# Optimization experiments

Measured on AMD Instinct MI355X. Metric: run time of the kernel, lower is better.

## Reference

```python
import jax, jax.numpy as jnp
import numpy as np

N_NODES = 100000
N_EDGES = 1600000
FEAT = 128
HID = 128
CLASSES = 10
GRAPHS = 64


def gcn_conv(x, W, b, src, dst, n):
    # PyG GCNConv: h = x @ W; add self-loops; symmetric deg^{-1/2} norm; scatter-add; + bias
    h = x @ W
    src_f = jnp.concatenate([src, jnp.arange(n, dtype=src.dtype)])
    dst_f = jnp.concatenate([dst, jnp.arange(n, dtype=dst.dtype)])
    deg = jax.ops.segment_sum(jnp.ones_like(dst_f, dtype=h.dtype), dst_f, num_segments=n)
    dinv = jax.lax.rsqrt(jnp.where(deg > 0, deg, 1.0))
    norm = dinv[src_f] * dinv[dst_f]              # [E+N]
    msg = h[src_f] * norm[:, None]                # gather + scale
    out = jax.ops.segment_sum(msg, dst_f, num_segments=n)  # scatter-add
    return out + b


def global_mean_pool(x, batch, num_graphs):
    s = jax.ops.segment_sum(x, batch, num_segments=num_graphs)
    cnt = jax.ops.segment_sum(jnp.ones_like(batch, dtype=x.dtype), batch, num_segments=num_graphs)
    return s / jnp.maximum(cnt, 1.0)[:, None]


def setup_inputs() -> dict:
    key = jax.random.key(0)
    ks = jax.random.split(key, 10)
    x = jax.random.normal(ks[0], (N_NODES, FEAT), dtype=jnp.float32)
    edge_index = jax.random.randint(ks[1], (2, N_EDGES), 0, N_NODES, dtype=jnp.int64)
    batch = jnp.sort(jax.random.randint(ks[2], (N_NODES,), 0, GRAPHS, dtype=jnp.int64))
    def glorot(k, fi, fo):
        s = float(np.sqrt(6.0 / (fi + fo)))
        return jax.random.uniform(k, (fi, fo), jnp.float32, -s, s)
    return {
        "x": x, "edge_index": edge_index, "batch": batch,
        "W1": glorot(ks[3], FEAT, HID), "b1": jnp.zeros((HID,), jnp.float32),
        "W2": glorot(ks[4], HID, HID), "b2": jnp.zeros((HID,), jnp.float32),
        "W3": glorot(ks[5], HID, HID), "b3": jnp.zeros((HID,), jnp.float32),
        "Wlin": glorot(ks[6], HID, CLASSES), "blin": jnp.zeros((CLASSES,), jnp.float32),
    }


def reference(x, edge_index, batch, W1, b1, W2, b2, W3, b3, Wlin, blin):
    src, dst = edge_index[0], edge_index[1]
    n = x.shape[0]
    h = jax.nn.relu(gcn_conv(x, W1, b1, src, dst, n))
    h = jax.nn.relu(gcn_conv(h, W2, b2, src, dst, n))
    h = gcn_conv(h, W3, b3, src, dst, n)
    emb = global_mean_pool(h, batch, GRAPHS)      # [GRAPHS, HID]
    # dropout(p=0.5) is identity in eval mode
    logits = emb @ Wlin + blin                    # [GRAPHS, CLASSES]
    return logits, jnp.squeeze(emb)
```

## Files before the change

kernel.cpp:

```cpp
#include <hip/hip_runtime.h>
#include <hip/hip_bf16.h>
#include <stdint.h>

typedef unsigned int uint32;
typedef __attribute__((ext_vector_type(8))) short short8;
typedef __attribute__((ext_vector_type(4))) float float4v;
typedef __attribute__((ext_vector_type(2))) float f32x2;

#define FEAT 128
#define NGRAPH 64
#define GB   256
#define NBK  512
#define QPG  8

__device__ __forceinline__ float bf2f_lo(uint32 v) {
    union { uint32 i; float f; } u; u.i = v << 16; return u.f;
}
__device__ __forceinline__ float bf2f_hi(uint32 v) {
    union { uint32 i; float f; } u; u.i = v & 0xffff0000u; return u.f;
}
__device__ __forceinline__ unsigned short f2bf(float f) {
    uint32 u = __builtin_bit_cast(uint32, f);
    uint32 r = (u + 0x7fffu + ((u >> 16) & 1u)) >> 16;
    return (unsigned short)r;
}
__device__ __forceinline__ uint32 f2bf2(float lo, float hi) {
    return (uint32)f2bf(lo) | ((uint32)f2bf(hi) << 16);
}

__global__ void k_bhist(const int* __restrict__ dst, int* __restrict__ bhistT,
                        const float* __restrict__ W1, const float* __restrict__ W2,
                        const float* __restrict__ W3, unsigned short* __restrict__ o1,
                        unsigned short* __restrict__ o2, unsigned short* __restrict__ o3,
                        int E) {
    int t = threadIdx.x, blk = blockIdx.x;
    if (blk >= GB) {
        int b2 = blk - GB;
        int wid = b2 >> 3;
        const float* W = (wid == 0) ? W1 : (wid == 1) ? W2 : W3;
        unsigned short* out = (wid == 0) ? o1 : (wid == 1) ? o2 : o3;
        int e = (b2 & 7) * 256 + t;
        int kt = e >> 9, ct = (e >> 6) & 7, lane = e & 63;
        int krow = kt * 32 + (lane >> 4) * 8;
        int col = ct * 16 + (lane & 15);
#pragma unroll
        for (int j = 0; j < 8; j++)
            out[e * 8 + j] = f2bf(W[(krow + j) * FEAT + col]);
        return;
    }
    __shared__ int h[NBK];
    for (int b = t; b < NBK; b += 256) h[b] = 0;
    __syncthreads();
    int chunk = (E + GB - 1) / GB;
    int lo = blk * chunk, hi = min(lo + chunk, E);
    for (int e = lo + t; e < hi; e += 256)
        atomicAdd(&h[dst[e] >> 8], 1);
    __syncthreads();
    for (int b = t; b < NBK; b += 256) bhistT[b * GB + blk] = h[b];
}

__global__ void k_boffs_a(int* __restrict__ bhistT, int* __restrict__ btot) {
    int b = blockIdx.x, l = threadIdx.x;
    int v[4];
    int base = b * GB + l * 4;
#pragma unroll
    for (int j = 0; j < 4; j++) v[j] = bhistT[base + j];
    int s = v[0] + v[1] + v[2] + v[3];
    int incl = s;
    for (int off = 1; off < 64; off <<= 1) {
        int u = __shfl_up(incl, off);
        if (l >= off) incl += u;
    }
    int excl = incl - s;
    int p0 = excl, p1 = p0 + v[0], p2 = p1 + v[1], p3 = p2 + v[2];
    bhistT[base + 0] = p0; bhistT[base + 1] = p1;
    bhistT[base + 2] = p2; bhistT[base + 3] = p3;
    if (l == 63) btot[b] = incl;
}

__global__ void k_boffs_b(const int* __restrict__ btot, int* __restrict__ bbase) {
    __shared__ int sc[NBK];
    int t = threadIdx.x;
    int s = btot[t];
    sc[t] = s;
    __syncthreads();
    for (int off = 1; off < NBK; off <<= 1) {
        int v = (t >= off) ? sc[t - off] : 0;
        __syncthreads();
        sc[t] += v;
        __syncthreads();
    }
    bbase[t] = sc[t] - s;
    if (t == NBK - 1) bbase[NBK] = sc[t];
}

__global__ void k_bscat(const int* __restrict__ src, const int* __restrict__ dst,
                        const int* __restrict__ bhistT, const int* __restrict__ bbase,
                        uint32* __restrict__ ebuf, int E) {
    __shared__ int cur[NBK];
    int t = threadIdx.x, blk = blockIdx.x;
    for (int b = t; b < NBK; b += 256) cur[b] = bbase[b] + bhistT[b * GB + blk];
    __syncthreads();
    int chunk = (E + GB - 1) / GB;
    int lo = blk * chunk, hi = min(lo + chunk, E);
    for (int e = lo + t; e < hi; e += 256) {
        int d = dst[e], s = src[e];
        int b = d >> 8;
        int p = atomicAdd(&cur[b], 1);
        ebuf[p] = ((uint32)s << 8) | (uint32)(d & 255);
    }
}

__global__ void k_csr(const uint32* __restrict__ ebuf, const int* __restrict__ bbase,
                      float* __restrict__ dinv, int* __restrict__ rowp,
                      int* __restrict__ csrc, int N, int E) {
    __shared__ int h[256];
    __shared__ int cur[256];
    int t = threadIdx.x, b = blockIdx.x;
    h[t] = 0;
    __syncthreads();
    int e0 = bbase[b], e1 = bbase[b + 1];
    for (int e = e0 + t; e < e1; e += 256)
        atomicAdd(&h[ebuf[e] & 255u], 1);
    __syncthreads();
    int deg = h[t];
    cur[t] = deg;
    __syncthreads();
    for (int off = 1; off < 256; off <<= 1) {
        int v = (t >= off) ? cur[t - off] : 0;
        __syncthreads();
        cur[t] += v;
        __syncthreads();
    }
    int r = bbase[b] + cur[t] - deg;
    int node = b * 256 + t;
    if (node < N) {
        rowp[node] = r;
        dinv[node] = rsqrtf((float)deg + 1.0f);
    }
    if (b == 0 && t == 0) rowp[N] = E;
    cur[t] = r;
    __syncthreads();
    for (int e = e0 + t; e < e1; e += 256) {
        uint32 v = ebuf[e];
        int p = atomicAdd(&cur[v & 255u], 1);
        csrc[p] = (int)(v >> 8);
    }
}

template <bool F32IN>
__global__ void k_gemm(const void* __restrict__ Xp,
                       const unsigned short* __restrict__ Wswz,
                       const float* __restrict__ dinv,
                       unsigned short* __restrict__ Hb, int N) {
    __shared__ unsigned short Wl[FEAT * FEAT];
    {
        const uint4* Wg = (const uint4*)Wswz;
        uint4* Ws = (uint4*)Wl;
        for (int i = threadIdx.x; i < 2048; i += 256) Ws[i] = Wg[i];
    }
    __syncthreads();

    int wave = threadIdx.x >> 6, lane = threadIdx.x & 63;
    int r0 = (blockIdx.x * 4 + wave) * 16;
    if (r0 >= N) return;
    int m = lane & 15, q = lane >> 4;

    int arow = r0 + m; if (arow >= N) arow = N - 1;
    short8 a[4];
    if (F32IN) {
        const float* Ar = (const float*)Xp + (long)arow * FEAT;
#pragma unroll
        for (int kt = 0; kt < 4; kt++) {
            float4 u = *(const float4*)(Ar + kt * 32 + q * 8);
            float4 v = *(const float4*)(Ar + kt * 32 + q * 8 + 4);
            short8 tv;
            tv[0] = (short)f2bf(u.x); tv[1] = (short)f2bf(u.y);
            tv[2] = (short)f2bf(u.z); tv[3] = (short)f2bf(u.w);
            tv[4] = (short)f2bf(v.x); tv[5] = (short)f2bf(v.y);
            tv[6] = (short)f2bf(v.z); tv[7] = (short)f2bf(v.w);
            a[kt] = tv;
        }
    } else {
        const short8* Ar = (const short8*)((const unsigned short*)Xp + (long)arow * FEAT);
#pragma unroll
        for (int kt = 0; kt < 4; kt++) a[kt] = Ar[kt * 4 + q];
    }

    const short8* Bl = (const short8*)Wl;
    float4v acc[8];
#pragma unroll
    for (int ct = 0; ct < 8; ct++) acc[ct] = (float4v){0.f, 0.f, 0.f, 0.f};
#pragma unroll
    for (int ct = 0; ct < 8; ct++) {
        acc[ct] = __builtin_amdgcn_mfma_f32_16x16x32_bf16(Bl[(0 * 8 + ct) * 64 + lane], a[0], acc[ct], 0, 0, 0);
        acc[ct] = __builtin_amdgcn_mfma_f32_16x16x32_bf16(Bl[(1 * 8 + ct) * 64 + lane], a[1], acc[ct], 0, 0, 0);
        acc[ct] = __builtin_amdgcn_mfma_f32_16x16x32_bf16(Bl[(2 * 8 + ct) * 64 + lane], a[2], acc[ct], 0, 0, 0);
        acc[ct] = __builtin_amdgcn_mfma_f32_16x16x32_bf16(Bl[(3 * 8 + ct) * 64 + lane], a[3], acc[ct], 0, 0, 0);
    }

    int node = r0 + m;
    bool ok = (node < N);
    float d = ok ? dinv[node] : 0.f;
#pragma unroll
    for (int ct = 0; ct < 8; ct++) {
        if (ok) {
            uint2 o;
            o.x = f2bf2(acc[ct][0] * d, acc[ct][1] * d);
            o.y = f2bf2(acc[ct][2] * d, acc[ct][3] * d);
            ((uint2*)(Hb + (long)node * FEAT + ct * 16))[q] = o;
        }
    }
}

template <int RELU>
__global__ void k_agg(const uint32* __restrict__ Hb,
                      const int* __restrict__ rowp, const int* __restrict__ csrc,
                      const float* __restrict__ dinv, const float* __restrict__ bias,
                      uint32* __restrict__ OUTb, int N) {
    int wave = threadIdx.x >> 6, lane = threadIdx.x & 63;
    int i = blockIdx.x * 4 + wave;
    if (i >= N) return;
    int f = lane & 15, quarter = lane >> 4;
    const uint4* H4 = (const uint4*)Hb;
    f32x2 c0 = {0.f, 0.f}, c1 = c0, c2 = c0, c3 = c0;
    int e0 = rowp[i], e1 = rowp[i + 1];
    int e = e0;
    for (; e + 16 <= e1; e += 16) {
        int  s[4];
        uint4 h[4];
#pragma unroll
        for (int j = 0; j < 4; j++) s[j] = csrc[e + 4 * j + quarter];
#pragma unroll
        for (int j = 0; j < 4; j++) h[j] = H4[(long)s[j] * 16 + f];
#pragma unroll
        for (int j = 0; j < 4; j++) {
            f32x2 u;
            u.x = bf2f_lo(h[j].x); u.y = bf2f_hi(h[j].x); c0 += u;
            u.x = bf2f_lo(h[j].y); u.y = bf2f_hi(h[j].y); c1 += u;
            u.x = bf2f_lo(h[j].z); u.y = bf2f_hi(h[j].z); c2 += u;
            u.x = bf2f_lo(h[j].w); u.y = bf2f_hi(h[j].w); c3 += u;
        }
    }
    {
        int r = e1 - e;
        int  s[4];
        uint4 h[4];
#pragma unroll
        for (int j = 0; j < 4; j++) {
            int idx = 4 * j + quarter;
            if (idx < r) s[j] = csrc[e + idx];
        }
#pragma unroll
        for (int j = 0; j < 4; j++)
            if (4 * j + quarter < r) h[j] = H4[(long)s[j] * 16 + f];
#pragma unroll
        for (int j = 0; j < 4; j++)
            if (4 * j + quarter < r) {
                f32x2 u;
                u.x = bf2f_lo(h[j].x); u.y = bf2f_hi(h[j].x); c0 += u;
                u.x = bf2f_lo(h[j].y); u.y = bf2f_hi(h[j].y); c1 += u;
                u.x = bf2f_lo(h[j].z); u.y = bf2f_hi(h[j].z); c2 += u;
                u.x = bf2f_lo(h[j].w); u.y = bf2f_hi(h[j].w); c3 += u;
            }
    }
    c0.x += __shfl_xor(c0.x, 16); c0.y += __shfl_xor(c0.y, 16);
    c1.x += __shfl_xor(c1.x, 16); c1.y += __shfl_xor(c1.y, 16);
    c2.x += __shfl_xor(c2.x, 16); c2.y += __shfl_xor(c2.y, 16);
    c3.x += __shfl_xor(c3.x, 16); c3.y += __shfl_xor(c3.y, 16);
    c0.x += __shfl_xor(c0.x, 32); c0.y += __shfl_xor(c0.y, 32);
    c1.x += __shfl_xor(c1.x, 32); c1.y += __shfl_xor(c1.y, 32);
    c2.x += __shfl_xor(c2.x, 32); c2.y += __shfl_xor(c2.y, 32);
    c3.x += __shfl_xor(c3.x, 32); c3.y += __shfl_xor(c3.y, 32);
    if (quarter == 0) {
        uint4 hv = H4[(long)i * 16 + f];
        c0.x += bf2f_lo(hv.x); c0.y += bf2f_hi(hv.x);
        c1.x += bf2f_lo(hv.y); c1.y += bf2f_hi(hv.y);
        c2.x += bf2f_lo(hv.z); c2.y += bf2f_hi(hv.z);
        c3.x += bf2f_lo(hv.w); c3.y += bf2f_hi(hv.w);
        float di = dinv[i];
        const float4* b4 = (const float4*)bias;
        float4 bb0 = b4[2 * f], bb1 = b4[2 * f + 1];
        c0.x = c0.x * di + bb0.x; c0.y = c0.y * di + bb0.y;
        c1.x = c1.x * di + bb0.z; c1.y = c1.y * di + bb0.w;
        c2.x = c2.x * di + bb1.x; c2.y = c2.y * di + bb1.y;
        c3.x = c3.x * di + bb1.z; c3.y = c3.y * di + bb1.w;
        if (RELU) {
            c0.x = fmaxf(c0.x, 0.f); c0.y = fmaxf(c0.y, 0.f);
            c1.x = fmaxf(c1.x, 0.f); c1.y = fmaxf(c1.y, 0.f);
            c2.x = fmaxf(c2.x, 0.f); c2.y = fmaxf(c2.y, 0.f);
            c3.x = fmaxf(c3.x, 0.f); c3.y = fmaxf(c3.y, 0.f);
        }
        uint4 o;
        o.x = f2bf2(c0.x, c0.y);
        o.y = f2bf2(c1.x, c1.y);
        o.z = f2bf2(c2.x, c2.y);
        o.w = f2bf2(c3.x, c3.y);
        ((uint4*)OUTb)[(long)i * 16 + f] = o;
    }
}

__global__ void k_pool2(const uint32* __restrict__ Gb, const int* __restrict__ batch,
                        float* __restrict__ pool, int N) {
    __shared__ float spx[256], spy[256];
    int t = threadIdx.x;
    int g = blockIdx.x >> 3, qtr = blockIdx.x & (QPG - 1);
    int lo, hi;
    { int l = 0, h = N; while (l < h) { int m = (l + h) >> 1; if (batch[m] < g) l = m + 1; else h = m; } lo = l; }
    { int l = lo, h = N; while (l < h) { int m = (l + h) >> 1; if (batch[m] < g + 1) l = m + 1; else h = m; } hi = l; }
    int cnt = hi - lo;
    int chunk = (cnt + QPG - 1) / QPG;
    int lo2 = lo + qtr * chunk;
    int hi2 = min(lo2 + chunk, hi);
    int f = t & 63, sub = t >> 6;
    float ax = 0.f, ay = 0.f;
#pragma unroll 4
    for (int i = lo2 + sub; i < hi2; i += 4) {
        uint32 v = Gb[(long)i * 64 + f];
        ax += bf2f_lo(v); ay += bf2f_hi(v);
    }
    spx[t] = ax; spy[t] = ay;
    __syncthreads();
    if (t < 64) {
        float sx = spx[t] + spx[t + 64] + spx[t + 128] + spx[t + 192];
        float sy = spy[t] + spy[t + 64] + spy[t + 128] + spy[t + 192];
        float* pr = pool + ((size_t)qtr * NGRAPH + g) * FEAT;
        pr[2 * t]     = sx;
        pr[2 * t + 1] = sy;
    }
}

__global__ void k_final(const float* __restrict__ pool, const int* __restrict__ batch,
                        const float* __restrict__ Wlin, const float* __restrict__ blin,
                        float* __restrict__ out, int N) {
    __shared__ float es[FEAT];
    __shared__ int lohi[2];
    int g = blockIdx.x, t = threadIdx.x;
    if (t < 2) {
        int key = g + t;
        int lo = 0, hi = N;
        while (lo < hi) {
            int mid = (lo + hi) >> 1;
            if (batch[mid] < key) lo = mid + 1; else hi = mid;
        }
        lohi[t] = lo;
    }
    float s = 0.f;
#pragma unroll
    for (int r = 0; r < QPG; r++) s += pool[(r * NGRAPH + g) * FEAT + t];
    __syncthreads();
    float c = (float)max(lohi[1] - lohi[0], 1);
    float e = s / c;
    es[t] = e;
    out[NGRAPH * 10 + g * FEAT + t] = e;
    __syncthreads();
    if (t < 10) {
        float a = blin[t];
        for (int k = 0; k < FEAT; k++)
            a += es[k] * Wlin[k * 10 + t];
        out[g * 10 + t] = a;
    }
}

extern "C" void kernel_launch(void* const* d_in, const int* in_sizes, int n_in,
                              void* d_out, int out_size, void* d_ws, size_t ws_size,
                              hipStream_t stream) {
    const float* x    = (const float*)d_in[0];
    const int*   ei   = (const int*)d_in[1];
    const int*   batch= (const int*)d_in[2];
    const float* W1   = (const float*)d_in[3];
    const float* b1   = (const float*)d_in[4];
    const float* W2   = (const float*)d_in[5];
    const float* b2   = (const float*)d_in[6];
    const float* W3   = (const float*)d_in[7];
    const float* b3   = (const float*)d_in[8];
    const float* Wlin = (const float*)d_in[9];
    const float* blin = (const float*)d_in[10];

    const int N = in_sizes[2];
    const int E = in_sizes[1] / 2;
    const int* src = ei;
    const int* dst = ei + E;
    const int NB = (N + 255) >> 8;

    char* w = (char*)d_ws;
    auto take = [&](size_t bytes) {
        char* p = w;
        w += (bytes + 255) & ~(size_t)255;
        return p;
    };
    float*  dinv   = (float*) take((size_t)N * 4);
    int*    rowp   = (int*)   take((size_t)(N + 1) * 4);
    int*    csrc   = (int*)   take((size_t)E * 4);
    uint32* ebuf   = (uint32*)take((size_t)E * 4);
    int*    bhistT = (int*)   take((size_t)GB * NBK * 4);
    int*    btot   = (int*)   take((size_t)NBK * 4);
    int*    bbase  = (int*)   take((size_t)(NBK + 1) * 4);
    uint32* hbuf   = (uint32*)take((size_t)N * FEAT * 2);
    uint32* gbuf   = (uint32*)take((size_t)N * FEAT * 2);
    unsigned short* w1s = (unsigned short*)take(FEAT * FEAT * 2);
    unsigned short* w2s = (unsigned short*)take(FEAT * FEAT * 2);
    unsigned short* w3s = (unsigned short*)take(FEAT * FEAT * 2);
    float*  pool   = (float*) take((size_t)QPG * NGRAPH * FEAT * 4);
    (void)ws_size; (void)n_in; (void)out_size;

    k_bhist  <<<GB + 24, 256, 0, stream>>>(dst, bhistT,
                                           W1, W2, W3, w1s, w2s, w3s, E);
    k_boffs_a<<<NBK, 64, 0, stream>>>(bhistT, btot);
    k_boffs_b<<<1, NBK, 0, stream>>>(btot, bbase);
    k_bscat  <<<GB, 256, 0, stream>>>(src, dst, bhistT, bbase, ebuf, E);
    k_csr    <<<NB, 256, 0, stream>>>(ebuf, bbase, dinv, rowp, csrc, N, E);

    const int tile_blocks = (N + 63) / 64;
    const int agg_blocks  = (N + 3) / 4;

    k_gemm<true> <<<tile_blocks, 256, 0, stream>>>(x, w1s, dinv, (unsigned short*)hbuf, N);
    k_agg<1><<<agg_blocks, 256, 0, stream>>>(hbuf, rowp, csrc, dinv, b1, gbuf, N);
    k_gemm<false><<<tile_blocks, 256, 0, stream>>>(gbuf, w2s, dinv, (unsigned short*)hbuf, N);
    k_agg<1><<<agg_blocks, 256, 0, stream>>>(hbuf, rowp, csrc, dinv, b2, gbuf, N);
    k_gemm<false><<<tile_blocks, 256, 0, stream>>>(gbuf, w3s, dinv, (unsigned short*)hbuf, N);
    k_agg<0><<<agg_blocks, 256, 0, stream>>>(hbuf, rowp, csrc, dinv, b3, gbuf, N);

    k_pool2<<<NGRAPH * QPG, 256, 0, stream>>>(gbuf, batch, pool, N);
    k_final<<<NGRAPH, 128, 0, stream>>>(pool, batch, Wlin, blin, (float*)d_out, N);
}
```

Before: 399.0 us.

## Split GCN aggregation into two feature-half passes to shrink gather working set

Each aggregation kernel is split into two launches, each handling half of the 128 features (128 bytes per node row). Within a wave, 8 lanes cover a half row and 8 edges are processed in parallel, 32 edges per iteration. The aim is to halve the gathered feature footprint per pass so more of the source rows stay cached in L2/MALL during the random gathers. The cost is reading the CSR indices twice, an extra launch per layer, and shorter contiguous segments per gathered row.

New measurement: 475.7 us. 1.19x slower.

```diff
diff --git a/kernel.cpp b/kernel.cpp
--- a/kernel.cpp
+++ b/kernel.cpp
@@ -213,7 +213,7 @@
     }
 }
 
-template <int RELU>
+template <int RELU, int HALF>
 __global__ void k_agg(const uint32* __restrict__ Hb,
                       const int* __restrict__ rowp, const int* __restrict__ csrc,
                       const float* __restrict__ dinv, const float* __restrict__ bias,
@@ -221,18 +221,18 @@
     int wave = threadIdx.x >> 6, lane = threadIdx.x & 63;
     int i = blockIdx.x * 4 + wave;
     if (i >= N) return;
-    int f = lane & 15, quarter = lane >> 4;
+    int f = lane & 7, oct = lane >> 3;
     const uint4* H4 = (const uint4*)Hb;
     f32x2 c0 = {0.f, 0.f}, c1 = c0, c2 = c0, c3 = c0;
     int e0 = rowp[i], e1 = rowp[i + 1];
     int e = e0;
-    for (; e + 16 <= e1; e += 16) {
+    for (; e + 32 <= e1; e += 32) {
         int  s[4];
         uint4 h[4];
 #pragma unroll
-        for (int j = 0; j < 4; j++) s[j] = csrc[e + 4 * j + quarter];
-#pragma unroll
-        for (int j = 0; j < 4; j++) h[j] = H4[(long)s[j] * 16 + f];
+        for (int j = 0; j < 4; j++) s[j] = csrc[e + 8 * j + oct];
+#pragma unroll
+        for (int j = 0; j < 4; j++) h[j] = H4[(long)s[j] * 16 + HALF * 8 + f];
 #pragma unroll
         for (int j = 0; j < 4; j++) {
             f32x2 u;
@@ -248,15 +248,15 @@
         uint4 h[4];
 #pragma unroll
         for (int j = 0; j < 4; j++) {
-            int idx = 4 * j + quarter;
+            int idx = 8 * j + oct;
             if (idx < r) s[j] = csrc[e + idx];
         }
 #pragma unroll
         for (int j = 0; j < 4; j++)
-            if (4 * j + quarter < r) h[j] = H4[(long)s[j] * 16 + f];
+            if (8 * j + oct < r) h[j] = H4[(long)s[j] * 16 + HALF * 8 + f];
 #pragma unroll
         for (int j = 0; j < 4; j++)
-            if (4 * j + quarter < r) {
+            if (8 * j + oct < r) {
                 f32x2 u;
                 u.x = bf2f_lo(h[j].x); u.y = bf2f_hi(h[j].x); c0 += u;
                 u.x = bf2f_lo(h[j].y); u.y = bf2f_hi(h[j].y); c1 += u;
@@ -264,23 +264,22 @@
                 u.x = bf2f_lo(h[j].w); u.y = bf2f_hi(h[j].w); c3 += u;
             }
     }
-    c0.x += __shfl_xor(c0.x, 16); c0.y += __shfl_xor(c0.y, 16);
-    c1.x += __shfl_xor(c1.x, 16); c1.y += __shfl_xor(c1.y, 16);
-    c2.x += __shfl_xor(c2.x, 16); c2.y += __shfl_xor(c2.y, 16);
-    c3.x += __shfl_xor(c3.x, 16); c3.y += __shfl_xor(c3.y, 16);
-    c0.x += __shfl_xor(c0.x, 32); c0.y += __shfl_xor(c0.y, 32);
-    c1.x += __shfl_xor(c1.x, 32); c1.y += __shfl_xor(c1.y, 32);
-    c2.x += __shfl_xor(c2.x, 32); c2.y += __shfl_xor(c2.y, 32);
-    c3.x += __shfl_xor(c3.x, 32); c3.y += __shfl_xor(c3.y, 32);
-    if (quarter == 0) {
-        uint4 hv = H4[(long)i * 16 + f];
+#pragma unroll
+    for (int d = 8; d <= 32; d <<= 1) {
+        c0.x += __shfl_xor(c0.x, d); c0.y += __shfl_xor(c0.y, d);
+        c1.x += __shfl_xor(c1.x, d); c1.y += __shfl_xor(c1.y, d);
+        c2.x += __shfl_xor(c2.x, d); c2.y += __shfl_xor(c2.y, d);
+        c3.x += __shfl_xor(c3.x, d); c3.y += __shfl_xor(c3.y, d);
+    }
+    if (oct == 0) {
+        uint4 hv = H4[(long)i * 16 + HALF * 8 + f];
         c0.x += bf2f_lo(hv.x); c0.y += bf2f_hi(hv.x);
         c1.x += bf2f_lo(hv.y); c1.y += bf2f_hi(hv.y);
         c2.x += bf2f_lo(hv.z); c2.y += bf2f_hi(hv.z);
         c3.x += bf2f_lo(hv.w); c3.y += bf2f_hi(hv.w);
         float di = dinv[i];
         const float4* b4 = (const float4*)bias;
-        float4 bb0 = b4[2 * f], bb1 = b4[2 * f + 1];
+        float4 bb0 = b4[HALF * 16 + 2 * f], bb1 = b4[HALF * 16 + 2 * f + 1];
         c0.x = c0.x * di + bb0.x; c0.y = c0.y * di + bb0.y;
         c1.x = c1.x * di + bb0.z; c1.y = c1.y * di + bb0.w;
         c2.x = c2.x * di + bb1.x; c2.y = c2.y * di + bb1.y;
@@ -296,7 +295,7 @@
         o.y = f2bf2(c1.x, c1.y);
         o.z = f2bf2(c2.x, c2.y);
         o.w = f2bf2(c3.x, c3.y);
-        ((uint4*)OUTb)[(long)i * 16 + f] = o;
+        ((uint4*)OUTb)[(long)i * 16 + HALF * 8 + f] = o;
     }
 }
 
@@ -415,11 +414,14 @@
     const int agg_blocks  = (N + 3) / 4;
 
     k_gemm<true> <<<tile_blocks, 256, 0, stream>>>(x, w1s, dinv, (unsigned short*)hbuf, N);
-    k_agg<1><<<agg_blocks, 256, 0, stream>>>(hbuf, rowp, csrc, dinv, b1, gbuf, N);
+    k_agg<1, 0><<<agg_blocks, 256, 0, stream>>>(hbuf, rowp, csrc, dinv, b1, gbuf, N);
+    k_agg<1, 1><<<agg_blocks, 256, 0, stream>>>(hbuf, rowp, csrc, dinv, b1, gbuf, N);
     k_gemm<false><<<tile_blocks, 256, 0, stream>>>(gbuf, w2s, dinv, (unsigned short*)hbuf, N);
-    k_agg<1><<<agg_blocks, 256, 0, stream>>>(hbuf, rowp, csrc, dinv, b2, gbuf, N);
+    k_agg<1, 0><<<agg_blocks, 256, 0, stream>>>(hbuf, rowp, csrc, dinv, b2, gbuf, N);
+    k_agg<1, 1><<<agg_blocks, 256, 0, stream>>>(hbuf, rowp, csrc, dinv, b2, gbuf, N);
     k_gemm<false><<<tile_blocks, 256, 0, stream>>>(gbuf, w3s, dinv, (unsigned short*)hbuf, N);
-    k_agg<0><<<agg_blocks, 256, 0, stream>>>(hbuf, rowp, csrc, dinv, b3, gbuf, N);
+    k_agg<0, 0><<<agg_blocks, 256, 0, stream>>>(hbuf, rowp, csrc, dinv, b3, gbuf, N);
+    k_agg<0, 1><<<agg_blocks, 256, 0, stream>>>(hbuf, rowp, csrc, dinv, b3, gbuf, N);
 
     k_pool2<<<NGRAPH * QPG, 256, 0, stream>>>(gbuf, batch, pool, N);
     k_final<<<NGRAPH, 128, 0, stream>>>(pool, batch, Wlin, blin, (float*)d_out, N);
```

## Fold bucket-offset scan into consumers and make GEMM grid persistent

Applied to the files above, without the earlier changes.

Removes the single-block k_boffs_b launch: k_bscat now scans the 512 bucket totals redundantly in each block, and k_csr computes its own base offset by reducing the preceding bucket totals. The GEMM kernels become grid-stride over tiles with the grid capped at 512 blocks, so the 32KB weight matrix is loaded into LDS fewer times in total. This saves one kernel launch and repeated weight staging, but adds redundant scan work per block, an O(NB) reduction per CSR block, and may reduce parallelism for the GEMMs.

After: 398.7 us. About the same (-0.1%).

```diff
diff --git a/kernel.cpp b/kernel.cpp
--- a/kernel.cpp
+++ b/kernel.cpp
@@ -78,28 +78,23 @@
     if (l == 63) btot[b] = incl;
 }
 
-__global__ void k_boffs_b(const int* __restrict__ btot, int* __restrict__ bbase) {
-    __shared__ int sc[NBK];
-    int t = threadIdx.x;
-    int s = btot[t];
-    sc[t] = s;
-    __syncthreads();
-    for (int off = 1; off < NBK; off <<= 1) {
-        int v = (t >= off) ? sc[t - off] : 0;
-        __syncthreads();
-        sc[t] += v;
-        __syncthreads();
-    }
-    bbase[t] = sc[t] - s;
-    if (t == NBK - 1) bbase[NBK] = sc[t];
-}
-
 __global__ void k_bscat(const int* __restrict__ src, const int* __restrict__ dst,
-                        const int* __restrict__ bhistT, const int* __restrict__ bbase,
+                        const int* __restrict__ bhistT, const int* __restrict__ btot,
                         uint32* __restrict__ ebuf, int E) {
     __shared__ int cur[NBK];
     int t = threadIdx.x, blk = blockIdx.x;
-    for (int b = t; b < NBK; b += 256) cur[b] = bbase[b] + bhistT[b * GB + blk];
+    int o0 = btot[t], o1 = btot[t + 256];
+    cur[t] = o0; cur[t + 256] = o1;
+    __syncthreads();
+    for (int off = 1; off < NBK; off <<= 1) {
+        int v0 = (t >= off) ? cur[t - off] : 0;
+        int v1 = (t + 256 >= off) ? cur[t + 256 - off] : 0;
+        __syncthreads();
+        cur[t] += v0; cur[t + 256] += v1;
+        __syncthreads();
+    }
+    cur[t]       = cur[t]       - o0 + bhistT[t * GB + blk];
+    cur[t + 256] = cur[t + 256] - o1 + bhistT[(t + 256) * GB + blk];
     __syncthreads();
     int chunk = (E + GB - 1) / GB;
     int lo = blk * chunk, hi = min(lo + chunk, E);
@@ -111,15 +106,26 @@
     }
 }
 
-__global__ void k_csr(const uint32* __restrict__ ebuf, const int* __restrict__ bbase,
+__global__ void k_csr(const uint32* __restrict__ ebuf, const int* __restrict__ btot,
                       float* __restrict__ dinv, int* __restrict__ rowp,
                       int* __restrict__ csrc, int N, int E) {
     __shared__ int h[256];
     __shared__ int cur[256];
+    __shared__ int ebase;
     int t = threadIdx.x, b = blockIdx.x;
+    int part = 0;
+    for (int j = t; j < b; j += 256) part += btot[j];
+    cur[t] = part;
+    __syncthreads();
+    for (int off = 128; off > 0; off >>= 1) {
+        if (t < off) cur[t] += cur[t + off];
+        __syncthreads();
+    }
+    if (t == 0) ebase = cur[0];
+    __syncthreads();
+    int e0 = ebase, e1 = e0 + btot[b];
     h[t] = 0;
     __syncthreads();
-    int e0 = bbase[b], e1 = bbase[b + 1];
     for (int e = e0 + t; e < e1; e += 256)
         atomicAdd(&h[ebuf[e] & 255u], 1);
     __syncthreads();
@@ -132,7 +138,7 @@
         cur[t] += v;
         __syncthreads();
     }
-    int r = bbase[b] + cur[t] - deg;
+    int r = e0 + cur[t] - deg;
     int node = b * 256 + t;
     if (node < N) {
         rowp[node] = r;
@@ -152,7 +158,7 @@
 __global__ void k_gemm(const void* __restrict__ Xp,
                        const unsigned short* __restrict__ Wswz,
                        const float* __restrict__ dinv,
-                       unsigned short* __restrict__ Hb, int N) {
+                       unsigned short* __restrict__ Hb, int N, int ntiles) {
     __shared__ unsigned short Wl[FEAT * FEAT];
     {
         const uint4* Wg = (const uint4*)Wswz;
@@ -162,53 +168,56 @@
     __syncthreads();
 
     int wave = threadIdx.x >> 6, lane = threadIdx.x & 63;
-    int r0 = (blockIdx.x * 4 + wave) * 16;
-    if (r0 >= N) return;
     int m = lane & 15, q = lane >> 4;
-
-    int arow = r0 + m; if (arow >= N) arow = N - 1;
-    short8 a[4];
-    if (F32IN) {
-        const float* Ar = (const float*)Xp + (long)arow * FEAT;
-#pragma unroll
-        for (int kt = 0; kt < 4; kt++) {
-            float4 u = *(const float4*)(Ar + kt * 32 + q * 8);
-            float4 v = *(const float4*)(Ar + kt * 32 + q * 8 + 4);
-            short8 tv;
-            tv[0] = (short)f2bf(u.x); tv[1] = (short)f2bf(u.y);
-            tv[2] = (short)f2bf(u.z); tv[3] = (short)f2bf(u.w);
-            tv[4] = (short)f2bf(v.x); tv[5] = (short)f2bf(v.y);
-            tv[6] = (short)f2bf(v.z); tv[7] = (short)f2bf(v.w);
-            a[kt] = tv;
-        }
-    } else {
-        const short8* Ar = (const short8*)((const unsigned short*)Xp + (long)arow * FEAT);
-#pragma unroll
-        for (int kt = 0; kt < 4; kt++) a[kt] = Ar[kt * 4 + q];
-    }
-
     const short8* Bl = (const short8*)Wl;
-    float4v acc[8];
-#pragma unroll
-    for (int ct = 0; ct < 8; ct++) acc[ct] = (float4v){0.f, 0.f, 0.f, 0.f};
-#pragma unroll
-    for (int ct = 0; ct < 8; ct++) {
-        acc[ct] = __builtin_amdgcn_mfma_f32_16x16x32_bf16(Bl[(0 * 8 + ct) * 64 + lane], a[0], acc[ct], 0, 0, 0);
-        acc[ct] = __builtin_amdgcn_mfma_f32_16x16x32_bf16(Bl[(1 * 8 + ct) * 64 + lane], a[1], acc[ct], 0, 0, 0);
-        acc[ct] = __builtin_amdgcn_mfma_f32_16x16x32_bf16(Bl[(2 * 8 + ct) * 64 + lane], a[2], acc[ct], 0, 0, 0);
-        acc[ct] = __builtin_amdgcn_mfma_f32_16x16x32_bf16(Bl[(3 * 8 + ct) * 64 + lane], a[3], acc[ct], 0, 0, 0);
-    }
-
-    int node = r0 + m;
-    bool ok = (node < N);
-    float d = ok ? dinv[node] : 0.f;
-#pragma unroll
-    for (int ct = 0; ct < 8; ct++) {
-        if (ok) {
-            uint2 o;
-            o.x = f2bf2(acc[ct][0] * d, acc[ct][1] * d);
-            o.y = f2bf2(acc[ct][2] * d, acc[ct][3] * d);
-            ((uint2*)(Hb + (long)node * FEAT + ct * 16))[q] = o;
+
+    for (int tb = blockIdx.x; tb < ntiles; tb += gridDim.x) {
+        int r0 = (tb * 4 + wave) * 16;
+        if (r0 >= N) continue;
+
+        int arow = r0 + m; if (arow >= N) arow = N - 1;
+        short8 a[4];
+        if (F32IN) {
+            const float* Ar = (const float*)Xp + (long)arow * FEAT;
+#pragma unroll
+            for (int kt = 0; kt < 4; kt++) {
+                float4 u = *(const float4*)(Ar + kt * 32 + q * 8);
+                float4 v = *(const float4*)(Ar + kt * 32 + q * 8 + 4);
+                short8 tv;
+                tv[0] = (short)f2bf(u.x); tv[1] = (short)f2bf(u.y);
+                tv[2] = (short)f2bf(u.z); tv[3] = (short)f2bf(u.w);
+                tv[4] = (short)f2bf(v.x); tv[5] = (short)f2bf(v.y);
+                tv[6] = (short)f2bf(v.z); tv[7] = (short)f2bf(v.w);
+                a[kt] = tv;
+            }
+        } else {
+            const short8* Ar = (const short8*)((const unsigned short*)Xp + (long)arow * FEAT);
+#pragma unroll
+            for (int kt = 0; kt < 4; kt++) a[kt] = Ar[kt * 4 + q];
+        }
+
+        float4v acc[8];
+#pragma unroll
+        for (int ct = 0; ct < 8; ct++) acc[ct] = (float4v){0.f, 0.f, 0.f, 0.f};
+#pragma unroll
+        for (int ct = 0; ct < 8; ct++) {
+            acc[ct] = __builtin_amdgcn_mfma_f32_16x16x32_bf16(Bl[(0 * 8 + ct) * 64 + lane], a[0], acc[ct], 0, 0, 0);
+            acc[ct] = __builtin_amdgcn_mfma_f32_16x16x32_bf16(Bl[(1 * 8 + ct) * 64 + lane], a[1], acc[ct], 0, 0, 0);
+            acc[ct] = __builtin_amdgcn_mfma_f32_16x16x32_bf16(Bl[(2 * 8 + ct) * 64 + lane], a[2], acc[ct], 0, 0, 0);
+            acc[ct] = __builtin_amdgcn_mfma_f32_16x16x32_bf16(Bl[(3 * 8 + ct) * 64 + lane], a[3], acc[ct], 0, 0, 0);
+        }
+
+        int node = r0 + m;
+        bool ok = (node < N);
+        float d = ok ? dinv[node] : 0.f;
+#pragma unroll
+        for (int ct = 0; ct < 8; ct++) {
+            if (ok) {
+                uint2 o;
+                o.x = f2bf2(acc[ct][0] * d, acc[ct][1] * d);
+                o.y = f2bf2(acc[ct][2] * d, acc[ct][3] * d);
+                ((uint2*)(Hb + (long)node * FEAT + ct * 16))[q] = o;
+            }
         }
     }
 }
@@ -395,7 +404,6 @@
     uint32* ebuf   = (uint32*)take((size_t)E * 4);
     int*    bhistT = (int*)   take((size_t)GB * NBK * 4);
     int*    btot   = (int*)   take((size_t)NBK * 4);
-    int*    bbase  = (int*)   take((size_t)(NBK + 1) * 4);
     uint32* hbuf   = (uint32*)take((size_t)N * FEAT * 2);
     uint32* gbuf   = (uint32*)take((size_t)N * FEAT * 2);
     unsigned short* w1s = (unsigned short*)take(FEAT * FEAT * 2);
@@ -407,18 +415,18 @@
     k_bhist  <<<GB + 24, 256, 0, stream>>>(dst, bhistT,
                                            W1, W2, W3, w1s, w2s, w3s, E);
     k_boffs_a<<<NBK, 64, 0, stream>>>(bhistT, btot);
-    k_boffs_b<<<1, NBK, 0, stream>>>(btot, bbase);
-    k_bscat  <<<GB, 256, 0, stream>>>(src, dst, bhistT, bbase, ebuf, E);
-    k_csr    <<<NB, 256, 0, stream>>>(ebuf, bbase, dinv, rowp, csrc, N, E);
+    k_bscat  <<<GB, 256, 0, stream>>>(src, dst, bhistT, btot, ebuf, E);
+    k_csr    <<<NB, 256, 0, stream>>>(ebuf, btot, dinv, rowp, csrc, N, E);
 
     const int tile_blocks = (N + 63) / 64;
     const int agg_blocks  = (N + 3) / 4;
-
-    k_gemm<true> <<<tile_blocks, 256, 0, stream>>>(x, w1s, dinv, (unsigned short*)hbuf, N);
+    const int gemm_grid   = (tile_blocks < 512) ? tile_blocks : 512;
+
+    k_gemm<true> <<<gemm_grid, 256, 0, stream>>>(x, w1s, dinv, (unsigned short*)hbuf, N, tile_blocks);
     k_agg<1><<<agg_blocks, 256, 0, stream>>>(hbuf, rowp, csrc, dinv, b1, gbuf, N);
-    k_gemm<false><<<tile_blocks, 256, 0, stream>>>(gbuf, w2s, dinv, (unsigned short*)hbuf, N);
+    k_gemm<false><<<gemm_grid, 256, 0, stream>>>(gbuf, w2s, dinv, (unsigned short*)hbuf, N, tile_blocks);
     k_agg<1><<<agg_blocks, 256, 0, stream>>>(hbuf, rowp, csrc, dinv, b2, gbuf, N);
-    k_gemm<false><<<tile_blocks, 256, 0, stream>>>(gbuf, w3s, dinv, (unsigned short*)hbuf, N);
+    k_gemm<false><<<gemm_grid, 256, 0, stream>>>(gbuf, w3s, dinv, (unsigned short*)hbuf, N, tile_blocks);
     k_agg<0><<<agg_blocks, 256, 0, stream>>>(hbuf, rowp, csrc, dinv, b3, gbuf, N);
 
     k_pool2<<<NGRAPH * QPG, 256, 0, stream>>>(gbuf, batch, pool, N);
```

## Replace prefix-scan bucketing with fixed-capacity atomic cursors and fuse pooling kernels

Applied to the files above, without the earlier changes.

The edge bucketing pass drops the global histogram, two prefix-scan kernels and the transposed histogram buffer. Each block instead reserves space in a fixed-capacity slot per bucket through a global atomic cursor. Row pointers become (start,end) pairs, and the pooling and final linear layer are merged into one 1024-thread kernel per graph. This removes several kernel launches and global passes, but it assumes no bucket holds more than CAP edges, which skewed graphs could overflow, and pooling now runs on only 64 blocks.

New measurement: 394.0 us, median of 2. Within noise of the previous version (-1.3%).

```diff
diff --git a/kernel.cpp b/kernel.cpp
--- a/kernel.cpp
+++ b/kernel.cpp
@@ -11,7 +11,6 @@
 #define NGRAPH 64
 #define GB   256
 #define NBK  512
-#define QPG  8
 
 __device__ __forceinline__ float bf2f_lo(uint32 v) {
     union { uint32 i; float f; } u; u.i = v << 16; return u.f;
@@ -28,27 +27,30 @@
     return (uint32)f2bf(lo) | ((uint32)f2bf(hi) << 16);
 }
 
-__global__ void k_bhist(const int* __restrict__ dst, int* __restrict__ bhistT,
-                        const float* __restrict__ W1, const float* __restrict__ W2,
-                        const float* __restrict__ W3, unsigned short* __restrict__ o1,
-                        unsigned short* __restrict__ o2, unsigned short* __restrict__ o3,
-                        int E) {
+__global__ void k_wswz(const float* __restrict__ W1, const float* __restrict__ W2,
+                       const float* __restrict__ W3, unsigned short* __restrict__ o1,
+                       unsigned short* __restrict__ o2, unsigned short* __restrict__ o3,
+                       int* __restrict__ cursor, int CAP) {
     int t = threadIdx.x, blk = blockIdx.x;
-    if (blk >= GB) {
-        int b2 = blk - GB;
-        int wid = b2 >> 3;
-        const float* W = (wid == 0) ? W1 : (wid == 1) ? W2 : W3;
-        unsigned short* out = (wid == 0) ? o1 : (wid == 1) ? o2 : o3;
-        int e = (b2 & 7) * 256 + t;
-        int kt = e >> 9, ct = (e >> 6) & 7, lane = e & 63;
-        int krow = kt * 32 + (lane >> 4) * 8;
-        int col = ct * 16 + (lane & 15);
-#pragma unroll
-        for (int j = 0; j < 8; j++)
-            out[e * 8 + j] = f2bf(W[(krow + j) * FEAT + col]);
-        return;
-    }
+    if (blk == 0)
+        for (int b = t; b < NBK; b += 256) cursor[b] = b * CAP;
+    int wid = blk >> 3;
+    const float* W = (wid == 0) ? W1 : (wid == 1) ? W2 : W3;
+    unsigned short* out = (wid == 0) ? o1 : (wid == 1) ? o2 : o3;
+    int e = (blk & 7) * 256 + t;
+    int kt = e >> 9, ct = (e >> 6) & 7, lane = e & 63;
+    int krow = kt * 32 + (lane >> 4) * 8;
+    int col = ct * 16 + (lane & 15);
+#pragma unroll
+    for (int j = 0; j < 8; j++)
+        out[e * 8 + j] = f2bf(W[(krow + j) * FEAT + col]);
+}
+
+__global__ void k_bscat2(const int* __restrict__ src, const int* __restrict__ dst,
+                         int* __restrict__ cursor, uint32* __restrict__ ebuf, int E) {
     __shared__ int h[NBK];
+    __shared__ int cur[NBK];
+    int t = threadIdx.x, blk = blockIdx.x;
     for (int b = t; b < NBK; b += 256) h[b] = 0;
     __syncthreads();
     int chunk = (E + GB - 1) / GB;
@@ -56,70 +58,28 @@
     for (int e = lo + t; e < hi; e += 256)
         atomicAdd(&h[dst[e] >> 8], 1);
     __syncthreads();
-    for (int b = t; b < NBK; b += 256) bhistT[b * GB + blk] = h[b];
-}
-
-__global__ void k_boffs_a(int* __restrict__ bhistT, int* __restrict__ btot) {
-    int b = blockIdx.x, l = threadIdx.x;
-    int v[4];
-    int base = b * GB + l * 4;
-#pragma unroll
-    for (int j = 0; j < 4; j++) v[j] = bhistT[base + j];
-    int s = v[0] + v[1] + v[2] + v[3];
-    int incl = s;
-    for (int off = 1; off < 64; off <<= 1) {
-        int u = __shfl_up(incl, off);
-        if (l >= off) incl += u;
-    }
-    int excl = incl - s;
-    int p0 = excl, p1 = p0 + v[0], p2 = p1 + v[1], p3 = p2 + v[2];
-    bhistT[base + 0] = p0; bhistT[base + 1] = p1;
-    bhistT[base + 2] = p2; bhistT[base + 3] = p3;
-    if (l == 63) btot[b] = incl;
-}
-
-__global__ void k_boffs_b(const int* __restrict__ btot, int* __restrict__ bbase) {
-    __shared__ int sc[NBK];
-    int t = threadIdx.x;
-    int s = btot[t];
-    sc[t] = s;
-    __syncthreads();
-    for (int off = 1; off < NBK; off <<= 1) {
-        int v = (t >= off) ? sc[t - off] : 0;
-        __syncthreads();
-        sc[t] += v;
-        __syncthreads();
-    }
-    bbase[t] = sc[t] - s;
-    if (t == NBK - 1) bbase[NBK] = sc[t];
-}
-
-__global__ void k_bscat(const int* __restrict__ src, const int* __restrict__ dst,
-                        const int* __restrict__ bhistT, const int* __restrict__ bbase,
-                        uint32* __restrict__ ebuf, int E) {
-    __shared__ int cur[NBK];
-    int t = threadIdx.x, blk = blockIdx.x;
-    for (int b = t; b < NBK; b += 256) cur[b] = bbase[b] + bhistT[b * GB + blk];
-    __syncthreads();
-    int chunk = (E + GB - 1) / GB;
-    int lo = blk * chunk, hi = min(lo + chunk, E);
+    for (int b = t; b < NBK; b += 256) {
+        int c = h[b];
+        cur[b] = c ? atomicAdd(&cursor[b], c) : 0;
+    }
+    __syncthreads();
     for (int e = lo + t; e < hi; e += 256) {
         int d = dst[e], s = src[e];
-        int b = d >> 8;
-        int p = atomicAdd(&cur[b], 1);
+        int p = atomicAdd(&cur[d >> 8], 1);
         ebuf[p] = ((uint32)s << 8) | (uint32)(d & 255);
     }
 }
 
-__global__ void k_csr(const uint32* __restrict__ ebuf, const int* __restrict__ bbase,
-                      float* __restrict__ dinv, int* __restrict__ rowp,
-                      int* __restrict__ csrc, int N, int E) {
+__global__ void k_csr2(const uint32* __restrict__ ebuf, const int* __restrict__ cursor,
+                       float* __restrict__ dinv, int2* __restrict__ rowp2,
+                       int* __restrict__ csrc, int N, int CAP) {
     __shared__ int h[256];
     __shared__ int cur[256];
     int t = threadIdx.x, b = blockIdx.x;
+    int e0 = b * CAP;
+    int e1 = cursor[b];
     h[t] = 0;
     __syncthreads();
-    int e0 = bbase[b], e1 = bbase[b + 1];
     for (int e = e0 + t; e < e1; e += 256)
         atomicAdd(&h[ebuf[e] & 255u], 1);
     __syncthreads();
@@ -132,13 +92,12 @@
         cur[t] += v;
         __syncthreads();
     }
-    int r = bbase[b] + cur[t] - deg;
+    int r = e0 + cur[t] - deg;
     int node = b * 256 + t;
     if (node < N) {
-        rowp[node] = r;
+        rowp2[node] = make_int2(r, r + deg);
         dinv[node] = rsqrtf((float)deg + 1.0f);
     }
-    if (b == 0 && t == 0) rowp[N] = E;
     cur[t] = r;
     __syncthreads();
     for (int e = e0 + t; e < e1; e += 256) {
@@ -215,7 +174,7 @@
 
 template <int RELU>
 __global__ void k_agg(const uint32* __restrict__ Hb,
-                      const int* __restrict__ rowp, const int* __restrict__ csrc,
+                      const int2* __restrict__ rowp2, const int* __restrict__ csrc,
                       const float* __restrict__ dinv, const float* __restrict__ bias,
                       uint32* __restrict__ OUTb, int N) {
     int wave = threadIdx.x >> 6, lane = threadIdx.x & 63;
@@ -224,7 +183,8 @@
     int f = lane & 15, quarter = lane >> 4;
     const uint4* H4 = (const uint4*)Hb;
     f32x2 c0 = {0.f, 0.f}, c1 = c0, c2 = c0, c3 = c0;
-    int e0 = rowp[i], e1 = rowp[i + 1];
+    int2 rr = rowp2[i];
+    int e0 = rr.x, e1 = rr.y;
     int e = e0;
     for (; e + 16 <= e1; e += 16) {
         int  s[4];
@@ -300,59 +260,34 @@
     }
 }
 
-__global__ void k_pool2(const uint32* __restrict__ Gb, const int* __restrict__ batch,
-                        float* __restrict__ pool, int N) {
-    __shared__ float spx[256], spy[256];
-    int t = threadIdx.x;
-    int g = blockIdx.x >> 3, qtr = blockIdx.x & (QPG - 1);
+__global__ void k_pf(const uint32* __restrict__ Gb, const int* __restrict__ batch,
+                     const float* __restrict__ Wlin, const float* __restrict__ blin,
+                     float* __restrict__ out, int N) {
+    __shared__ float spx[1024], spy[1024];
+    __shared__ float es[FEAT];
+    int t = threadIdx.x, g = blockIdx.x;
     int lo, hi;
     { int l = 0, h = N; while (l < h) { int m = (l + h) >> 1; if (batch[m] < g) l = m + 1; else h = m; } lo = l; }
     { int l = lo, h = N; while (l < h) { int m = (l + h) >> 1; if (batch[m] < g + 1) l = m + 1; else h = m; } hi = l; }
-    int cnt = hi - lo;
-    int chunk = (cnt + QPG - 1) / QPG;
-    int lo2 = lo + qtr * chunk;
-    int hi2 = min(lo2 + chunk, hi);
     int f = t & 63, sub = t >> 6;
     float ax = 0.f, ay = 0.f;
 #pragma unroll 4
-    for (int i = lo2 + sub; i < hi2; i += 4) {
+    for (int i = lo + sub; i < hi; i += 16) {
         uint32 v = Gb[(long)i * 64 + f];
         ax += bf2f_lo(v); ay += bf2f_hi(v);
     }
     spx[t] = ax; spy[t] = ay;
     __syncthreads();
     if (t < 64) {
-        float sx = spx[t] + spx[t + 64] + spx[t + 128] + spx[t + 192];
-        float sy = spy[t] + spy[t + 64] + spy[t + 128] + spy[t + 192];
-        float* pr = pool + ((size_t)qtr * NGRAPH + g) * FEAT;
-        pr[2 * t]     = sx;
-        pr[2 * t + 1] = sy;
-    }
-}
-
-__global__ void k_final(const float* __restrict__ pool, const int* __restrict__ batch,
-                        const float* __restrict__ Wlin, const float* __restrict__ blin,
-                        float* __restrict__ out, int N) {
-    __shared__ float es[FEAT];
-    __shared__ int lohi[2];
-    int g = blockIdx.x, t = threadIdx.x;
-    if (t < 2) {
-        int key = g + t;
-        int lo = 0, hi = N;
-        while (lo < hi) {
-            int mid = (lo + hi) >> 1;
-            if (batch[mid] < key) lo = mid + 1; else hi = mid;
-        }
-        lohi[t] = lo;
-    }
-    float s = 0.f;
-#pragma unroll
-    for (int r = 0; r < QPG; r++) s += pool[(r * NGRAPH + g) * FEAT + t];
-    __syncthreads();
-    float c = (float)max(lohi[1] - lohi[0], 1);
-    float e = s / c;
-    es[t] = e;
-    out[NGRAPH * 10 + g * FEAT + t] = e;
+        float sx = 0.f, sy = 0.f;
+#pragma unroll
+        for (int r = 0; r < 16; r++) { sx += spx[t + 64 * r]; sy += spy[t + 64 * r]; }
+        float c = (float)max(hi - lo, 1);
+        float e0 = sx / c, e1 = sy / c;
+        es[2 * t] = e0; es[2 * t + 1] = e1;
+        out[NGRAPH * 10 + g * FEAT + 2 * t]     = e0;
+        out[NGRAPH * 10 + g * FEAT + 2 * t + 1] = e1;
+    }
     __syncthreads();
     if (t < 10) {
         float a = blin[t];
@@ -382,6 +317,8 @@
     const int* src = ei;
     const int* dst = ei + E;
     const int NB = (N + 255) >> 8;
+    int CAP = ((E * 2 / (NB > 0 ? NB : 1)) + 255) & ~255;
+    if (CAP < 1024) CAP = 1024;
 
     char* w = (char*)d_ws;
     auto take = [&](size_t bytes) {
@@ -390,37 +327,30 @@
         return p;
     };
     float*  dinv   = (float*) take((size_t)N * 4);
-    int*    rowp   = (int*)   take((size_t)(N + 1) * 4);
-    int*    csrc   = (int*)   take((size_t)E * 4);
-    uint32* ebuf   = (uint32*)take((size_t)E * 4);
-    int*    bhistT = (int*)   take((size_t)GB * NBK * 4);
-    int*    btot   = (int*)   take((size_t)NBK * 4);
-    int*    bbase  = (int*)   take((size_t)(NBK + 1) * 4);
+    int2*   rowp2  = (int2*)  take((size_t)N * 8);
+    int*    csrc   = (int*)   take((size_t)NB * CAP * 4);
+    uint32* ebuf   = (uint32*)take((size_t)NB * CAP * 4);
+    int*    cursor = (int*)   take((size_t)NBK * 4);
     uint32* hbuf   = (uint32*)take((size_t)N * FEAT * 2);
     uint32* gbuf   = (uint32*)take((size_t)N * FEAT * 2);
     unsigned short* w1s = (unsigned short*)take(FEAT * FEAT * 2);
     unsigned short* w2s = (unsigned short*)take(FEAT * FEAT * 2);
     unsigned short* w3s = (unsigned short*)take(FEAT * FEAT * 2);
-    float*  pool   = (float*) take((size_t)QPG * NGRAPH * FEAT * 4);
     (void)ws_size; (void)n_in; (void)out_size;
 
-    k_bhist  <<<GB + 24, 256, 0, stream>>>(dst, bhistT,
-                                           W1, W2, W3, w1s, w2s, w3s, E);
-    k_boffs_a<<<NBK, 64, 0, stream>>>(bhistT, btot);
-    k_boffs_b<<<1, NBK, 0, stream>>>(btot, bbase);
-    k_bscat  <<<GB, 256, 0, stream>>>(src, dst, bhistT, bbase, ebuf, E);
-    k_csr    <<<NB, 256, 0, stream>>>(ebuf, bbase, dinv, rowp, csrc, N, E);
+    k_wswz  <<<24, 256, 0, stream>>>(W1, W2, W3, w1s, w2s, w3s, cursor, CAP);
+    k_bscat2<<<GB, 256, 0, stream>>>(src, dst, cursor, ebuf, E);
+    k_csr2  <<<NB, 256, 0, stream>>>(ebuf, cursor, dinv, rowp2, csrc, N, CAP);
 
     const int tile_blocks = (N + 63) / 64;
     const int agg_blocks  = (N + 3) / 4;
 
     k_gemm<true> <<<tile_blocks, 256, 0, stream>>>(x, w1s, dinv, (unsigned short*)hbuf, N);
-    k_agg<1><<<agg_blocks, 256, 0, stream>>>(hbuf, rowp, csrc, dinv, b1, gbuf, N);
+    k_agg<1><<<agg_blocks, 256, 0, stream>>>(hbuf, rowp2, csrc, dinv, b1, gbuf, N);
     k_gemm<false><<<tile_blocks, 256, 0, stream>>>(gbuf, w2s, dinv, (unsigned short*)hbuf, N);
-    k_agg<1><<<agg_blocks, 256, 0, stream>>>(hbuf, rowp, csrc, dinv, b2, gbuf, N);
+    k_agg<1><<<agg_blocks, 256, 0, stream>>>(hbuf, rowp2, csrc, dinv, b2, gbuf, N);
     k_gemm<false><<<tile_blocks, 256, 0, stream>>>(gbuf, w3s, dinv, (unsigned short*)hbuf, N);
-    k_agg<0><<<agg_blocks, 256, 0, stream>>>(hbuf, rowp, csrc, dinv, b3, gbuf, N);
-
-    k_pool2<<<NGRAPH * QPG, 256, 0, stream>>>(gbuf, batch, pool, N);
-    k_final<<<NGRAPH, 128, 0, stream>>>(pool, batch, Wlin, blin, (float*)d_out, N);
-}
+    k_agg<0><<<agg_blocks, 256, 0, stream>>>(hbuf, rowp2, csrc, dinv, b3, gbuf, N);
+
+    k_pf<<<NGRAPH, 1024, 0, stream>>>(gbuf, batch, Wlin, blin, (float*)d_out, N);
+}
```
